# Kernel optimization log

Hardware: AMD Instinct MI355X
Metric: run time of the kernel (lower is better)

## Reference

```python
import jax, jax.numpy as jnp
import numpy as np

BATCH, H, NFAM = 32768, 1024, 10


def setup_inputs() -> dict:
    key = jax.random.key(0)
    k1, k2, k3, k4 = jax.random.split(key, 4)
    scale1 = 1.0 / np.sqrt(2 * H)
    scale2 = 1.0 / np.sqrt(H)
    return {
        "features": jax.random.normal(k1, (BATCH, H), dtype=jnp.float32),
        "prototypes": jax.random.normal(k2, (NFAM, H), dtype=jnp.float32),
        "W1": jax.random.normal(k3, (2 * H, H), dtype=jnp.float32) * scale1,
        "b1": jnp.zeros((H,), dtype=jnp.float32),
        "W2": jax.random.normal(k4, (H, H), dtype=jnp.float32) * scale2,
        "b2": jnp.zeros((H,), dtype=jnp.float32),
    }


def reference(features, prototypes, W1, b1, W2, b2):
    # Squared euclidean distances via the norm trick (avoids [B, NFAM, H] blowup).
    # argmin over squared distances == argmin over cdist (sqrt is monotone).
    f2 = jnp.sum(features * features, axis=1, keepdims=True)        # [B, 1]
    p2 = jnp.sum(prototypes * prototypes, axis=1)                   # [NFAM]
    d2 = f2 + p2[None, :] - 2.0 * (features @ prototypes.T)         # [B, NFAM]
    nearest_idx = jnp.argmin(d2, axis=1)                            # [B]
    nearest_prototypes = prototypes[nearest_idx]                    # [B, H]
    combined = jnp.concatenate([features, nearest_prototypes], axis=1)  # [B, 2H]
    hidden = jax.nn.relu(combined @ W1 + b1)                        # [B, H]
    adapted = hidden @ W2 + b2                                      # [B, H]
    return adapted
```

## Files before the change

### kernel.cpp

```cpp
#include <hip/hip_runtime.h>
#include <stdint.h>
#include <stddef.h>

#define BATCH 32768
#define HDIM  1024
#define NFAM  10

typedef short bf16x8 __attribute__((ext_vector_type(8)));
typedef float f32x4  __attribute__((ext_vector_type(4)));

__device__ __forceinline__ unsigned short f2bf(float x) {
  unsigned int u = __builtin_bit_cast(unsigned int, x);
  u += 0x7fffu + ((u >> 16) & 1u);
  return (unsigned short)(u >> 16);
}

__device__ __forceinline__ void async_cp16(unsigned short* lds_dst, const unsigned short* g_src) {
  __builtin_amdgcn_global_load_lds(
      (const __attribute__((address_space(1))) unsigned int*)g_src,
      (__attribute__((address_space(3))) unsigned int*)lds_dst,
      16, 0, 0);
}

__global__ __launch_bounds__(256) void transpose_cast(
    const float* __restrict__ in, unsigned short* __restrict__ out, int R, int C) {
  __shared__ float tile[64][65];
  const int t = threadIdx.x;
  const int c = t & 63;
  const int r0 = t >> 6;
  const int rbase = blockIdx.y * 64, cbase = blockIdx.x * 64;
#pragma unroll
  for (int i = 0; i < 16; ++i) {
    int r = r0 + i * 4;
    tile[r][c] = in[(size_t)(rbase + r) * C + cbase + c];
  }
  __syncthreads();
#pragma unroll
  for (int i = 0; i < 16; ++i) {
    int r = r0 + i * 4;
    out[(size_t)(cbase + r) * R + rbase + c] = f2bf(tile[c][r]);
  }
}

__global__ __launch_bounds__(256) void proto_prep(
    const float* __restrict__ protos, float* __restrict__ p2) {
  __shared__ float red[4];
  const int j = blockIdx.x, t = threadIdx.x;
  float4 v = ((const float4*)(protos + (size_t)j * HDIM))[t];
  float s = v.x * v.x + v.y * v.y + v.z * v.z + v.w * v.w;
#pragma unroll
  for (int o = 32; o > 0; o >>= 1) s += __shfl_down(s, o);
  if ((t & 63) == 0) red[t >> 6] = s;
  __syncthreads();
  if (t == 0) p2[j] = red[0] + red[1] + red[2] + red[3];
}

__global__ __launch_bounds__(256) void proto_contrib(
    const float* __restrict__ protos, const float* __restrict__ W1,
    const float* __restrict__ b1, float* __restrict__ protoC) {
  __shared__ float red[4][64];
  const int j  = blockIdx.y;
  const int ln = threadIdx.x & 63;
  const int ks = threadIdx.x >> 6;
  const int n  = blockIdx.x * 64 + ln;
  const float* p = protos + (size_t)j * HDIM + ks * 256;
  const float* w = W1 + (size_t)(HDIM + ks * 256) * HDIM + n;
  float s = 0.f;
#pragma unroll 16
  for (int kk = 0; kk < 256; ++kk)
    s += p[kk] * w[(size_t)kk * HDIM];
  red[ks][ln] = s;
  __syncthreads();
  if (ks == 0)
    protoC[j * HDIM + n] = red[0][ln] + red[1][ln] + red[2][ln] + red[3][ln] + b1[n];
}

__global__ __launch_bounds__(256) void nearest_kernel(
    const float* __restrict__ feats, const float* __restrict__ protos,
    const float* __restrict__ p2, unsigned short* __restrict__ featsB,
    int* __restrict__ idx) {
  __shared__ float pl[NFAM * HDIM];
  const int t = threadIdx.x;
#pragma unroll
  for (int j = 0; j < NFAM; ++j)
    ((float4*)pl)[t + 256 * j] = ((const float4*)protos)[t + 256 * j];
  __syncthreads();

  const int wave = t >> 6, lane = t & 63;
  float P2[NFAM];
#pragma unroll
  for (int j = 0; j < NFAM; ++j) P2[j] = p2[j];

#pragma unroll
  for (int rr = 0; rr < 4; ++rr) {
    const int row = blockIdx.x * 16 + wave * 4 + rr;
    const float* f = feats + (size_t)row * HDIM;

    float dot[NFAM];
#pragma unroll
    for (int j = 0; j < NFAM; ++j) dot[j] = 0.f;
    float f2 = 0.f;

#pragma unroll
    for (int ch = 0; ch < 4; ++ch) {
      const int k4 = ch * 64 + lane;
      float4 v = ((const float4*)f)[k4];
      f2 += v.x * v.x + v.y * v.y + v.z * v.z + v.w * v.w;
#pragma unroll
      for (int j = 0; j < NFAM; ++j) {
        float4 p = ((const float4*)pl)[j * 256 + k4];
        dot[j] += v.x * p.x + v.y * p.y + v.z * p.z + v.w * p.w;
      }
      uint2 pk;
      pk.x = (unsigned)f2bf(v.x) | ((unsigned)f2bf(v.y) << 16);
      pk.y = (unsigned)f2bf(v.z) | ((unsigned)f2bf(v.w) << 16);
      *(uint2*)(featsB + (size_t)row * HDIM + k4 * 4) = pk;
    }

#pragma unroll
    for (int o = 32; o > 0; o >>= 1) {
      f2 += __shfl_down(f2, o);
#pragma unroll
      for (int j = 0; j < NFAM; ++j) dot[j] += __shfl_down(dot[j], o);
    }
    if (lane == 0) {
      int best = 0;
      float bd = f2 + P2[0] - 2.f * dot[0];
#pragma unroll
      for (int j = 1; j < NFAM; ++j) {
        float d = f2 + P2[j] - 2.f * dot[j];
        if (d < bd) { bd = d; best = j; }
      }
      idx[row] = best;
    }
  }
}

template <int EPI>
__global__ __launch_bounds__(256) void gemm_kernel(
    const unsigned short* __restrict__ A,
    const unsigned short* __restrict__ Bt,
    const int* __restrict__ idx,
    const float* __restrict__ protoC,
    const float* __restrict__ bias,
    unsigned short* __restrict__ outB,
    float* __restrict__ outF) {
  constexpr int K = 1024;
  __shared__ unsigned short ldsA[2][2][128 * 32];
  __shared__ unsigned short ldsB[2][2][128 * 32];

  const int t    = threadIdx.x;
  const int lane = t & 63;
  const int wid  = t >> 6;
  const int quad = lane >> 4;
  const int r16  = lane & 15;

  const int b = blockIdx.x;
  const int rowBase = ((b >> 6) * 8 + (b & 7)) * 128;
  const int colBase = ((b >> 3) & 7) * 128;
  const int wm = (wid >> 1) * 64;
  const int wn = (wid & 1) * 64;

  f32x4 acc[4][4];
#pragma unroll
  for (int i = 0; i < 4; ++i)
#pragma unroll
    for (int j = 0; j < 4; ++j) acc[i][j] = (f32x4){0.f, 0.f, 0.f, 0.f};

  const int r0 = t >> 2, r1 = r0 + 64;
  const int q = (t & 3) ^ ((t >> 3) & 3);
  const unsigned short* aBase0 = A + (size_t)(rowBase + r0) * K + q * 8;
  const unsigned short* aBase1 = A + (size_t)(rowBase + r1) * K + q * 8;
  const unsigned short* bB0 = Bt + (size_t)(colBase + r0) * K + q * 8;
  const unsigned short* bB1 = Bt + (size_t)(colBase + r1) * K + q * 8;

  const int pr = quad ^ ((r16 >> 1) & 3);

#define ISSUE_TILE(buf, kb)                                        \
  {                                                                \
    _Pragma("unroll")                                              \
    for (int s = 0; s < 2; ++s) {                                  \
      async_cp16(&ldsA[buf][s][t * 8],         aBase0 + (kb) + s * 32); \
      async_cp16(&ldsA[buf][s][(t + 256) * 8], aBase1 + (kb) + s * 32); \
      async_cp16(&ldsB[buf][s][t * 8],         bB0 + (kb) + s * 32);    \
      async_cp16(&ldsB[buf][s][(t + 256) * 8], bB1 + (kb) + s * 32);    \
    }                                                              \
  }

  ISSUE_TILE(0, 0);
  int cur = 0;
  for (int kb = 0; kb < K; kb += 64) {
    if (kb + 64 < K) {
      ISSUE_TILE(cur ^ 1, kb + 64);
      asm volatile("s_waitcnt vmcnt(8)" ::: "memory");
    } else {
      asm volatile("s_waitcnt vmcnt(0)" ::: "memory");
    }
    __builtin_amdgcn_s_barrier();
    __builtin_amdgcn_sched_barrier(0);

#pragma unroll
    for (int s = 0; s < 2; ++s) {
      bf16x8 af[4], bfr[4];
#pragma unroll
      for (int mi = 0; mi < 4; ++mi)
        af[mi] = *(const bf16x8*)(&ldsA[cur][s][(wm + mi * 16 + r16) * 32 + pr * 8]);
#pragma unroll
      for (int ni = 0; ni < 4; ++ni)
        bfr[ni] = *(const bf16x8*)(&ldsB[cur][s][(wn + ni * 16 + r16) * 32 + pr * 8]);
#pragma unroll
      for (int mi = 0; mi < 4; ++mi)
#pragma unroll
        for (int ni = 0; ni < 4; ++ni)
          acc[mi][ni] = __builtin_amdgcn_mfma_f32_16x16x32_bf16(af[mi], bfr[ni], acc[mi][ni], 0, 0, 0);
    }

    __builtin_amdgcn_sched_barrier(0);
    __builtin_amdgcn_s_barrier();
    cur ^= 1;
  }
#undef ISSUE_TILE

#pragma unroll
  for (int mi = 0; mi < 4; ++mi) {
    const int lrow0 = wm + mi * 16 + quad * 4;
    const int grow0 = rowBase + lrow0;
    int pid[4];
    if (EPI) {
#pragma unroll
      for (int r = 0; r < 4; ++r) pid[r] = idx[grow0 + r];
    }
#pragma unroll
    for (int ni = 0; ni < 4; ++ni) {
      const int gcol = colBase + wn + ni * 16 + r16;
      if (EPI) {
#pragma unroll
        for (int r = 0; r < 4; ++r) {
          float v = acc[mi][ni][r] + protoC[(size_t)pid[r] * HDIM + gcol];
          v = fmaxf(v, 0.0f);
          outB[(size_t)(grow0 + r) * 1024 + gcol] = f2bf(v);
        }
      } else {
        const float bv = bias[gcol];
#pragma unroll
        for (int r = 0; r < 4; ++r)
          outF[(size_t)(grow0 + r) * 1024 + gcol] = acc[mi][ni][r] + bv;
      }
    }
  }
}

extern "C" void kernel_launch(void* const* d_in, const int* in_sizes, int n_in,
                              void* d_out, int out_size, void* d_ws, size_t ws_size,
                              hipStream_t stream) {
  const float* feats  = (const float*)d_in[0];
  const float* protos = (const float*)d_in[1];
  const float* W1     = (const float*)d_in[2];
  const float* b1     = (const float*)d_in[3];
  const float* W2     = (const float*)d_in[4];
  const float* b2     = (const float*)d_in[5];
  float* out = (float*)d_out;

  unsigned short* featsB  = (unsigned short*)d_ws;
  unsigned short* hiddenB = featsB + (size_t)BATCH * HDIM;
  unsigned short* W1t     = hiddenB + (size_t)BATCH * HDIM;
  unsigned short* W2t     = W1t + (size_t)HDIM * HDIM;
  float* protoC = (float*)(W2t + (size_t)HDIM * HDIM);
  float* p2     = protoC + NFAM * HDIM;
  int* idx      = (int*)(p2 + NFAM + 2);

  transpose_cast<<<dim3(HDIM / 64, HDIM / 64), 256, 0, stream>>>(W1, W1t, HDIM, HDIM);
  transpose_cast<<<dim3(HDIM / 64, HDIM / 64), 256, 0, stream>>>(W2, W2t, HDIM, HDIM);
  proto_prep<<<NFAM, 256, 0, stream>>>(protos, p2);
  proto_contrib<<<dim3(HDIM / 64, NFAM), 256, 0, stream>>>(protos, W1, b1, protoC);
  nearest_kernel<<<BATCH / 16, 256, 0, stream>>>(feats, protos, p2, featsB, idx);
  gemm_kernel<1><<<2048, 256, 0, stream>>>(featsB, W1t, idx, protoC, nullptr, hiddenB, nullptr);
  gemm_kernel<0><<<2048, 256, 0, stream>>>(hiddenB, W2t, nullptr, nullptr, b2, nullptr, out);
}
```

Before: 429.8 us.

## Switch GEMMs to 256x256 tiles with 8 waves and four-phase pipelined loads

Result: slower. 479.4 us (+11.5%).

```diff
diff --git a/kernel.cpp b/kernel.cpp
--- a/kernel.cpp
+++ b/kernel.cpp
@@ -137,7 +137,7 @@
 }
 
 template <int EPI>
-__global__ __launch_bounds__(256) void gemm_kernel(
+__global__ __launch_bounds__(512, 2) void gemm256(
     const unsigned short* __restrict__ A,
     const unsigned short* __restrict__ Bt,
     const int* __restrict__ idx,
@@ -145,106 +145,139 @@
     const float* __restrict__ bias,
     unsigned short* __restrict__ outB,
     float* __restrict__ outF) {
-  constexpr int K = 1024;
-  __shared__ unsigned short ldsA[2][2][128 * 32];
-  __shared__ unsigned short ldsB[2][2][128 * 32];
+  constexpr int K  = 1024;
+  constexpr int NT = K / 64;
+  __shared__ unsigned short ldsA[2 * 2 * 2 * 128 * 32];
+  __shared__ unsigned short ldsB[2 * 2 * 2 * 128 * 32];
 
   const int t    = threadIdx.x;
   const int lane = t & 63;
-  const int wid  = t >> 6;
   const int quad = lane >> 4;
   const int r16  = lane & 15;
+  const int wid  = t >> 6;
+  const int wm   = wid >> 2;
+  const int wn   = wid & 3;
 
   const int b = blockIdx.x;
-  const int rowBase = ((b >> 6) * 8 + (b & 7)) * 128;
-  const int colBase = ((b >> 3) & 7) * 128;
-  const int wm = (wid >> 1) * 64;
-  const int wn = (wid & 1) * 64;
-
-  f32x4 acc[4][4];
-#pragma unroll
-  for (int i = 0; i < 4; ++i)
-#pragma unroll
-    for (int j = 0; j < 4; ++j) acc[i][j] = (f32x4){0.f, 0.f, 0.f, 0.f};
-
-  const int r0 = t >> 2, r1 = r0 + 64;
-  const int q = (t & 3) ^ ((t >> 3) & 3);
-  const unsigned short* aBase0 = A + (size_t)(rowBase + r0) * K + q * 8;
-  const unsigned short* aBase1 = A + (size_t)(rowBase + r1) * K + q * 8;
-  const unsigned short* bB0 = Bt + (size_t)(colBase + r0) * K + q * 8;
-  const unsigned short* bB1 = Bt + (size_t)(colBase + r1) * K + q * 8;
+  const int rowBase = ((b >> 5) + (b & 7) * 16) * 256;
+  const int colBase = ((b >> 3) & 3) * 256;
+
+  const int sr = t >> 2;
+  const int q  = (t & 3) ^ ((t >> 3) & 3);
+  const unsigned short* pA = A  + (size_t)(rowBase + sr) * K + q * 8;
+  const unsigned short* pB = Bt + (size_t)(colBase + sr) * K + q * 8;
+  const int ldst = t * 8;
 
   const int pr = quad ^ ((r16 >> 1) & 3);
 
-#define ISSUE_TILE(buf, kb)                                        \
-  {                                                                \
-    _Pragma("unroll")                                              \
-    for (int s = 0; s < 2; ++s) {                                  \
-      async_cp16(&ldsA[buf][s][t * 8],         aBase0 + (kb) + s * 32); \
-      async_cp16(&ldsA[buf][s][(t + 256) * 8], aBase1 + (kb) + s * 32); \
-      async_cp16(&ldsB[buf][s][t * 8],         bB0 + (kb) + s * 32);    \
-      async_cp16(&ldsB[buf][s][(t + 256) * 8], bB1 + (kb) + s * 32);    \
-    }                                                              \
-  }
-
-  ISSUE_TILE(0, 0);
-  int cur = 0;
-  for (int kb = 0; kb < K; kb += 64) {
-    if (kb + 64 < K) {
-      ISSUE_TILE(cur ^ 1, kb + 64);
-      asm volatile("s_waitcnt vmcnt(8)" ::: "memory");
-    } else {
-      asm volatile("s_waitcnt vmcnt(0)" ::: "memory");
-    }
-    __builtin_amdgcn_s_barrier();
-    __builtin_amdgcn_sched_barrier(0);
-
-#pragma unroll
-    for (int s = 0; s < 2; ++s) {
-      bf16x8 af[4], bfr[4];
-#pragma unroll
-      for (int mi = 0; mi < 4; ++mi)
-        af[mi] = *(const bf16x8*)(&ldsA[cur][s][(wm + mi * 16 + r16) * 32 + pr * 8]);
-#pragma unroll
-      for (int ni = 0; ni < 4; ++ni)
-        bfr[ni] = *(const bf16x8*)(&ldsB[cur][s][(wn + ni * 16 + r16) * 32 + pr * 8]);
-#pragma unroll
-      for (int mi = 0; mi < 4; ++mi)
-#pragma unroll
-        for (int ni = 0; ni < 4; ++ni)
-          acc[mi][ni] = __builtin_amdgcn_mfma_f32_16x16x32_bf16(af[mi], bfr[ni], acc[mi][ni], 0, 0, 0);
-    }
-
-    __builtin_amdgcn_sched_barrier(0);
-    __builtin_amdgcn_s_barrier();
-    cur ^= 1;
-  }
-#undef ISSUE_TILE
-
-#pragma unroll
-  for (int mi = 0; mi < 4; ++mi) {
-    const int lrow0 = wm + mi * 16 + quad * 4;
-    const int grow0 = rowBase + lrow0;
-    int pid[4];
-    if (EPI) {
-#pragma unroll
-      for (int r = 0; r < 4; ++r) pid[r] = idx[grow0 + r];
-    }
-#pragma unroll
-    for (int ni = 0; ni < 4; ++ni) {
-      const int gcol = colBase + wn + ni * 16 + r16;
+  f32x4 acc[2][2][4][2];
+#pragma unroll
+  for (int a0 = 0; a0 < 2; ++a0)
+#pragma unroll
+    for (int b0 = 0; b0 < 2; ++b0)
+#pragma unroll
+      for (int m0 = 0; m0 < 4; ++m0)
+#pragma unroll
+        for (int n0 = 0; n0 < 2; ++n0) acc[a0][b0][m0][n0] = (f32x4){0.f, 0.f, 0.f, 0.f};
+
+#define STAGE_A(buf, h, kb)                                                        \
+  {                                                                                \
+    async_cp16(ldsA + (buf) * 16384 + (0 * 2 + (h)) * 4096 + ldst,                 \
+               pA + (size_t)(h) * (128 * K) + (kb) + 0 * 32);                      \
+    async_cp16(ldsA + (buf) * 16384 + (1 * 2 + (h)) * 4096 + ldst,                 \
+               pA + (size_t)(h) * (128 * K) + (kb) + 1 * 32);                      \
+  }
+#define STAGE_B(buf, h, kb)                                                        \
+  {                                                                                \
+    async_cp16(ldsB + (buf) * 16384 + (0 * 2 + (h)) * 4096 + ldst,                 \
+               pB + (size_t)(h) * (128 * K) + (kb) + 0 * 32);                      \
+    async_cp16(ldsB + (buf) * 16384 + (1 * 2 + (h)) * 4096 + ldst,                 \
+               pB + (size_t)(h) * (128 * K) + (kb) + 1 * 32);                      \
+  }
+
+  STAGE_A(0, 0, 0);
+  STAGE_B(0, 0, 0);
+  STAGE_A(0, 1, 0);
+  STAGE_B(0, 1, 0);
+
+  for (int kt = 0; kt < NT; ++kt) {
+    const int p   = kt & 1;
+    const int kbn = ((kt + 1) & (NT - 1)) * 64;
+#pragma unroll
+    for (int ph = 0; ph < 4; ++ph) {
+      if (ph == 0)      STAGE_A(p ^ 1, 0, kbn)
+      else if (ph == 1) STAGE_B(p ^ 1, 0, kbn)
+      else if (ph == 2) STAGE_A(p ^ 1, 1, kbn)
+      else              STAGE_B(p ^ 1, 1, kbn)
+
+      if (ph == 3) asm volatile("s_waitcnt vmcnt(8)" ::: "memory");
+      else         asm volatile("s_waitcnt vmcnt(6)" ::: "memory");
+      asm volatile("s_barrier" ::: "memory");
+      __builtin_amdgcn_sched_barrier(0);
+
+      const int ah = ph & 1;
+      const int bh = ph >> 1;
+
+      bf16x8 av[2][4], bv[2][2];
+#pragma unroll
+      for (int s = 0; s < 2; ++s)
+#pragma unroll
+        for (int mi = 0; mi < 4; ++mi)
+          av[s][mi] = *(const bf16x8*)(ldsA + p * 16384 + (s * 2 + ah) * 4096 +
+                                       (wm * 64 + mi * 16 + r16) * 32 + pr * 8);
+#pragma unroll
+      for (int s = 0; s < 2; ++s)
+#pragma unroll
+        for (int ni = 0; ni < 2; ++ni)
+          bv[s][ni] = *(const bf16x8*)(ldsB + p * 16384 + (s * 2 + bh) * 4096 +
+                                       (wn * 32 + ni * 16 + r16) * 32 + pr * 8);
+
+      __builtin_amdgcn_s_setprio(1);
+#pragma unroll
+      for (int s = 0; s < 2; ++s)
+#pragma unroll
+        for (int mi = 0; mi < 4; ++mi)
+#pragma unroll
+          for (int ni = 0; ni < 2; ++ni)
+            acc[ah][bh][mi][ni] = __builtin_amdgcn_mfma_f32_16x16x32_bf16(
+                av[s][mi], bv[s][ni], acc[ah][bh][mi][ni], 0, 0, 0);
+      __builtin_amdgcn_s_setprio(0);
+      __builtin_amdgcn_sched_barrier(0);
+      asm volatile("s_barrier" ::: "memory");
+    }
+  }
+#undef STAGE_A
+#undef STAGE_B
+
+#pragma unroll
+  for (int ah = 0; ah < 2; ++ah) {
+#pragma unroll
+    for (int mi = 0; mi < 4; ++mi) {
+      const int grow0 = rowBase + ah * 128 + wm * 64 + mi * 16 + quad * 4;
+      int pid[4];
       if (EPI) {
 #pragma unroll
-        for (int r = 0; r < 4; ++r) {
-          float v = acc[mi][ni][r] + protoC[(size_t)pid[r] * HDIM + gcol];
-          v = fmaxf(v, 0.0f);
-          outB[(size_t)(grow0 + r) * 1024 + gcol] = f2bf(v);
+        for (int r = 0; r < 4; ++r) pid[r] = idx[grow0 + r];
+      }
+#pragma unroll
+      for (int bh = 0; bh < 2; ++bh) {
+#pragma unroll
+        for (int ni = 0; ni < 2; ++ni) {
+          const int gcol = colBase + bh * 128 + wn * 32 + ni * 16 + r16;
+          if (EPI) {
+#pragma unroll
+            for (int r = 0; r < 4; ++r) {
+              float v = acc[ah][bh][mi][ni][r] + protoC[(size_t)pid[r] * HDIM + gcol];
+              v = fmaxf(v, 0.0f);
+              outB[(size_t)(grow0 + r) * 1024 + gcol] = f2bf(v);
+            }
+          } else {
+            const float bv = bias[gcol];
+#pragma unroll
+            for (int r = 0; r < 4; ++r)
+              outF[(size_t)(grow0 + r) * 1024 + gcol] = acc[ah][bh][mi][ni][r] + bv;
+          }
         }
-      } else {
-        const float bv = bias[gcol];
-#pragma unroll
-        for (int r = 0; r < 4; ++r)
-          outF[(size_t)(grow0 + r) * 1024 + gcol] = acc[mi][ni][r] + bv;
       }
     }
   }
@@ -274,6 +307,6 @@
   proto_prep<<<NFAM, 256, 0, stream>>>(protos, p2);
   proto_contrib<<<dim3(HDIM / 64, NFAM), 256, 0, stream>>>(protos, W1, b1, protoC);
   nearest_kernel<<<BATCH / 16, 256, 0, stream>>>(feats, protos, p2, featsB, idx);
-  gemm_kernel<1><<<2048, 256, 0, stream>>>(featsB, W1t, idx, protoC, nullptr, hiddenB, nullptr);
-  gemm_kernel<0><<<2048, 256, 0, stream>>>(hiddenB, W2t, nullptr, nullptr, b2, nullptr, out);
-}
+  gemm256<1><<<512, 512, 0, stream>>>(featsB, W1t, idx, protoC, nullptr, hiddenB, nullptr);
+  gemm256<0><<<512, 512, 0, stream>>>(hiddenB, W2t, nullptr, nullptr, b2, nullptr, out);
+}
```
